# Kernel optimization log

Measured on AMD Instinct MI355X. Metric: run time of the kernel, lower is better.

## Reference

```python
import jax, jax.numpy as jnp
import numpy as np
from functools import partial

B, C, H, W = 256, 3, 128, 128

def _conv(x, w, b, pad):
    y = jax.lax.conv_general_dilated(x, w, (1, 1), [(pad, pad), (pad, pad)],
                                     dimension_numbers=('NCHW', 'OIHW', 'NCHW'))
    return y + b[None, :, None, None]

def _maxpool2(x):
    return jax.lax.reduce_window(x, -jnp.inf, jax.lax.max, (1, 1, 2, 2), (1, 1, 2, 2), 'VALID')

def _linear(x, w, b):
    return x @ w.T + b

def _handcrafted(images):
    # uint8 quantization: floor(x*255); inputs in [0,1) so no wraparound
    img8 = jnp.floor(images * 255.0)                      # [B,3,H,W]
    brightness = img8.mean(axis=(-2, -1))                 # [B,3]
    contrast = img8.std(axis=(-2, -1))                    # [B,3] (ddof=0, numpy default)
    # cv2.Sobel ksize=3, BORDER_REFLECT_101 == jnp.pad 'reflect'; cv2 does correlation
    kx = jnp.array([[-1., 0., 1.], [-2., 0., 2.], [-1., 0., 1.]], dtype=img8.dtype)
    ky = kx.T
    k = jnp.stack([kx, ky])[:, None]                      # [2,1,3,3]
    p = jnp.pad(img8, ((0, 0), (0, 0), (1, 1), (1, 1)), mode='reflect')
    s = jax.lax.conv_general_dilated(p.reshape(B * 3, 1, H + 2, W + 2), k, (1, 1),
                                     'VALID', dimension_numbers=('NCHW', 'OIHW', 'NCHW'))
    edge = jnp.sqrt(s[:, 0] ** 2 + s[:, 1] ** 2).mean(axis=(-2, -1)).reshape(B, 3)
    return jnp.concatenate([edge, brightness, contrast], axis=1)  # [B,9]

def setup_inputs() -> dict:
    key = jax.random.key(0)
    ks = jax.random.split(key, 20)
    g = lambda i, shape, fan: (jax.random.normal(ks[i], shape, jnp.float32) * (1.0 / np.sqrt(fan)))
    return {
        'images': jax.random.uniform(ks[0], (B, C, H, W), jnp.float32),
        'W1': g(1, (32, 3, 3, 3), 27), 'b1': jnp.zeros((32,), jnp.float32),
        'W2': g(2, (64, 32, 3, 3), 288), 'b2': jnp.zeros((64,), jnp.float32),
        'Wa': g(3, (1, 64, 7, 7), 64 * 49), 'ba': jnp.zeros((1,), jnp.float32),
        'Wfc': g(4, (50, 64 * 32 * 32), 64 * 32 * 32), 'bfc': jnp.zeros((50,), jnp.float32),
        'Wh1': g(5, (32, 9), 9), 'bh1': jnp.zeros((32,), jnp.float32),
        'Wh2': g(6, (64, 32), 32), 'bh2': jnp.zeros((64,), jnp.float32),
        'Wh3': g(7, (50, 64), 64), 'bh3': jnp.zeros((50,), jnp.float32),
        'Wf': g(8, (64, 100), 100), 'bf': jnp.zeros((64,), jnp.float32),
        'Wc': g(9, (1, 64), 64), 'bc': jnp.zeros((1,), jnp.float32),
    }

def reference(images, W1, b1, W2, b2, Wa, ba, Wfc, bfc,
              Wh1, bh1, Wh2, bh2, Wh3, bh3, Wf, bf, Wc, bc):
    # CNN branch
    x = jax.nn.relu(_conv(images, W1, b1, 1))
    x = _maxpool2(x)
    x = jax.nn.relu(_conv(x, W2, b2, 1))
    x = _maxpool2(x)                                      # [B,64,32,32]
    attn = jax.nn.sigmoid(_conv(x, Wa, ba, 3))            # spatial attention
    x = x * attn
    cnn_feat = jax.nn.relu(_linear(x.reshape(B, -1), Wfc, bfc))  # [B,50]
    # handcrafted branch
    f = _handcrafted(images)                              # [B,9]
    h = jax.nn.relu(_linear(f, Wh1, bh1))
    h = jax.nn.relu(_linear(h, Wh2, bh2))
    h = jax.nn.relu(_linear(h, Wh3, bh3))                 # [B,50]
    fused = jax.nn.relu(_linear(jnp.concatenate([cnn_feat, h], axis=1), Wf, bf))
    logits = _linear(fused, Wc, bc)
    return jax.nn.sigmoid(logits)
```

## Files before the change

kernel.cpp:

```cpp
#include <hip/hip_runtime.h>
#include <stdint.h>

typedef __bf16 bf16x8 __attribute__((ext_vector_type(8)));
typedef float f32x4 __attribute__((ext_vector_type(4)));

__device__ inline float bf2f(uint16_t u) {
    uint32_t x = ((uint32_t)u) << 16;
    float f;
    __builtin_memcpy(&f, &x, 4);
    return f;
}
__device__ inline uint16_t f2bf(float f) {
    uint32_t x;
    __builtin_memcpy(&x, &f, 4);
    uint32_t r = (x + 0x7FFFu + ((x >> 16) & 1u)) >> 16;
    return (uint16_t)r;
}

__global__ __launch_bounds__(256) void k_prep_w2(const float* __restrict__ W2,
                                                 uint16_t* __restrict__ wA) {
    int j = blockIdx.x * 256 + threadIdx.x;
    if (j >= 18432) return;
    int t = j >> 11, rem = j & 2047, oc = rem >> 5, ic = rem & 31;
    int dy = t / 3, dx = t - dy * 3;
    wA[j] = f2bf(W2[(oc * 32 + ic) * 9 + dy * 3 + dx]);
}

__global__ __launch_bounds__(256) void k_prep_w1(const float* __restrict__ W1,
                                                 uint16_t* __restrict__ wA1c) {
    int j = blockIdx.x * 256 + threadIdx.x;
    if (j >= 3072) return;
    int dy = j >> 10, rem = j & 1023, oc = rem >> 5, k = rem & 31;
    int dx = k >> 2, ic = k & 3;
    uint16_t v = 0;
    if (dx < 3 && ic < 3) v = f2bf(W1[((oc * 3 + ic) * 3 + dy) * 3 + dx]);
    wA1c[j] = v;
}

__global__ __launch_bounds__(256) void k_prep_wa(const float* __restrict__ Wa,
                                                 uint16_t* __restrict__ waP) {
    int j = blockIdx.x * 256 + threadIdx.x;
    if (j >= 4096) return;
    int chunk = j >> 10, ks = (j >> 9) & 1, tl = (j >> 5) & 15, ch = j & 31;
    int t = chunk * 16 + tl;
    int cg = ks * 32 + ch;
    waP[j] = (t < 49) ? f2bf(Wa[cg * 49 + t]) : (uint16_t)0;
}

__global__ __launch_bounds__(256) void k_prep_wfc(const float* __restrict__ Wfc,
                                                  uint16_t* __restrict__ wfcb) {
    int o = blockIdx.x;
    int pb = blockIdx.y;
    int ch = threadIdx.x & 63;
    int pr = threadIdx.x >> 6;
    const float* src = Wfc + (size_t)o * 65536 + ch * 1024;
    uint16_t* dst = wfcb + (size_t)o * 65536 + ch;
#pragma unroll 4
    for (int i = 0; i < 16; ++i) {
        int px = pb * 64 + i * 4 + pr;
        dst[(size_t)px * 64] = f2bf(src[px]);
    }
}

__global__ __launch_bounds__(256) void k_handcrafted(const float* __restrict__ img,
                                                     float* __restrict__ f) {
    __shared__ float p[128 * 128];
    int c = blockIdx.x, b = blockIdx.y;
    const float* src = img + (((size_t)(b * 3 + c)) << 14);
    int tid = threadIdx.x;
    float sum = 0.f, sumsq = 0.f;
    for (int it = 0; it < 64; ++it) {
        int idx = tid + (it << 8);
        float v = floorf(src[idx] * 255.0f);
        p[idx] = v;
        sum += v;
        sumsq += v * v;
    }
    __syncthreads();
    float esum = 0.f;
    for (int it = 0; it < 64; ++it) {
        int idx = tid + (it << 8);
        int r = idx >> 7, cc = idx & 127;
        int rm = (r == 0) ? 1 : (r - 1), rp = (r == 127) ? 126 : (r + 1);
        int cm = (cc == 0) ? 1 : (cc - 1), cp = (cc == 127) ? 126 : (cc + 1);
        float a0 = p[(rm << 7) + cm], a1 = p[(rm << 7) + cc], a2 = p[(rm << 7) + cp];
        float b0 = p[(r << 7) + cm], b2 = p[(r << 7) + cp];
        float c0 = p[(rp << 7) + cm], c1 = p[(rp << 7) + cc], c2 = p[(rp << 7) + cp];
        float gx = (a2 - a0) + 2.f * (b2 - b0) + (c2 - c0);
        float gy = (c0 + 2.f * c1 + c2) - (a0 + 2.f * a1 + a2);
        esum += sqrtf(gx * gx + gy * gy);
    }
    for (int off = 32; off; off >>= 1) {
        sum += __shfl_down(sum, off);
        sumsq += __shfl_down(sumsq, off);
        esum += __shfl_down(esum, off);
    }
    __syncthreads();
    int w = tid >> 6;
    if ((tid & 63) == 0) {
        p[w * 3 + 0] = sum;
        p[w * 3 + 1] = sumsq;
        p[w * 3 + 2] = esum;
    }
    __syncthreads();
    if (tid == 0) {
        float S = 0.f, Q = 0.f, E = 0.f;
        for (int i = 0; i < 4; ++i) {
            S += p[i * 3 + 0];
            Q += p[i * 3 + 1];
            E += p[i * 3 + 2];
        }
        const float inv = 1.0f / 16384.0f;
        float mean = S * inv;
        float var = Q * inv - mean * mean;
        f[b * 16 + c] = E * inv;
        f[b * 16 + 3 + c] = mean;
        f[b * 16 + 6 + c] = sqrtf(fmaxf(var, 0.f));
    }
}

__global__ __launch_bounds__(256) void k_conv1_mfma(const float* __restrict__ img,
                                                    const uint16_t* __restrict__ wA1c,
                                                    const float* __restrict__ b1,
                                                    uint16_t* __restrict__ pooled1) {
    __shared__ uint16_t s_nhwc[18 * 34 * 4 + 32];
    __shared__ uint16_t s_out[8 * 16 * 32];
    const int tile = blockIdx.x;
    const int b = blockIdx.y;
    const int ty = tile >> 2, tx = tile & 3;
    const int Y0 = ty * 16, X0 = tx * 32;
    const int tid = threadIdx.x;

    for (int j = tid; j < 612; j += 256) {
        int r = j / 34, sc = j - r * 34;
        int gy = Y0 - 1 + r, gx = X0 - 1 + sc;
        uint16_t d[4] = {0, 0, 0, 0};
        if ((unsigned)gy < 128u && (unsigned)gx < 128u) {
            size_t base = (((size_t)b * 3) << 14) + (gy << 7) + gx;
#pragma unroll
            for (int ic = 0; ic < 3; ++ic) d[ic] = f2bf(img[base + ((size_t)ic << 14)]);
        }
        *(uint2*)&s_nhwc[j * 4] = *(uint2*)d;
    }

    const int wv = tid >> 6, lane = tid & 63;
    const int rowl = lane & 15, kg = lane >> 4;

    bf16x8 afr[3][2];
#pragma unroll
    for (int dy = 0; dy < 3; ++dy)
#pragma unroll
        for (int g = 0; g < 2; ++g)
            afr[dy][g] = *(const bf16x8*)(wA1c + dy * 1024 + (g * 16 + rowl) * 32 + kg * 8);
    float bias[2][4];
#pragma unroll
    for (int g = 0; g < 2; ++g)
#pragma unroll
        for (int r = 0; r < 4; ++r)
            bias[g][r] = b1[g * 16 + kg * 4 + r];

    __syncthreads();

#pragma unroll
    for (int pr = 0; pr < 2; ++pr) {
#pragma unroll
        for (int seg = 0; seg < 2; ++seg) {
            const int y0 = wv * 4 + pr * 2;
            const int xl = seg * 16 + rowl;
            bf16x8 bw[4];
#pragma unroll
            for (int rr = 0; rr < 4; ++rr) {
                const uint16_t* rp = &s_nhwc[((y0 + rr) * 34 + xl + kg * 2) * 4];
                uint2 lo = *(const uint2*)rp;
                uint2 hi = *(const uint2*)(rp + 4);
                union { uint2 u[2]; bf16x8 v; } u;
                u.u[0] = lo;
                u.u[1] = hi;
                bw[rr] = u.v;
            }
            f32x4 acc0[2], acc1[2];
#pragma unroll
            for (int g = 0; g < 2; ++g)
#pragma unroll
                for (int r = 0; r < 4; ++r) {
                    acc0[g][r] = bias[g][r];
                    acc1[g][r] = bias[g][r];
                }
#pragma unroll
            for (int dy = 0; dy < 3; ++dy)
#pragma unroll
                for (int g = 0; g < 2; ++g) {
                    acc0[g] = __builtin_amdgcn_mfma_f32_16x16x32_bf16(afr[dy][g], bw[dy], acc0[g], 0, 0, 0);
                    acc1[g] = __builtin_amdgcn_mfma_f32_16x16x32_bf16(afr[dy][g], bw[dy + 1], acc1[g], 0, 0, 0);
                }
#pragma unroll
            for (int g = 0; g < 2; ++g)
#pragma unroll
                for (int r = 0; r < 4; ++r) {
                    float m = fmaxf(acc0[g][r], acc1[g][r]);
                    m = fmaxf(m, 0.f);
                    float o = fmaxf(m, __shfl_xor(m, 1));
                    if (!(lane & 1)) {
                        int prow = wv * 2 + pr;
                        int pcol = seg * 8 + (rowl >> 1);
                        int oc = g * 16 + kg * 4 + r;
                        s_out[(prow * 16 + pcol) * 32 + oc] = f2bf(o);
                    }
                }
        }
    }
    __syncthreads();
    for (int u = tid; u < 512; u += 256) {
        int px = u >> 2, c = u & 3;
        int prow = px >> 4, pcol = px & 15;
        uint4 v = *(const uint4*)&s_out[px * 32 + c * 8];
        ((uint4*)pooled1)[((((size_t)b << 12) + (ty * 8 + prow) * 64 + tx * 16 + pcol) << 2) + c] = v;
    }
}

__global__ __launch_bounds__(256) void k_conv2_mfma(const uint16_t* __restrict__ pooled1,
                                                    const uint16_t* __restrict__ wA,
                                                    const float* __restrict__ b2v,
                                                    uint16_t* __restrict__ pooled2n) {
    __shared__ uint16_t s_in[10 * 34 * 32];
    __shared__ uint16_t s_out[64 * 64];
    const int bx = blockIdx.x;
    const int b = blockIdx.y;
    const int tx = bx >> 3, ty = bx & 7;
    const int X0 = tx * 32, Y0 = ty * 8;
    const int tid = threadIdx.x;

    for (int j = tid; j < 1360; j += 256) {
        int r = j / 136;
        int rem = j - r * 136;
        int px = rem >> 2, c4 = rem & 3;
        int gy = Y0 - 1 + r, gx = X0 - 1 + px;
        uint4 v = make_uint4(0, 0, 0, 0);
        if ((unsigned)gy < 64u && (unsigned)gx < 64u)
            v = ((const uint4*)pooled1)[((((size_t)b << 12) + gy * 64 + gx) << 2) + c4];
        *(uint4*)&s_in[(r * 34 + px) * 32 + c4 * 8] = v;
    }

    const int wv = tid >> 6, lane = tid & 63;
    const int ocq = wv & 1, xth = wv >> 1;
    const int rowl = lane & 15, kg = lane >> 4;

    bf16x8 afr[9][2];
#pragma unroll
    for (int t = 0; t < 9; ++t)
#pragma unroll
        for (int g = 0; g < 2; ++g)
            afr[t][g] = *(const bf16x8*)(wA + t * 2048 + (ocq * 32 + g * 16 + rowl) * 32 + kg * 8);
    float bias[2][4];
#pragma unroll
    for (int g = 0; g < 2; ++g)
#pragma unroll
        for (int r = 0; r < 4; ++r)
            bias[g][r] = b2v[ocq * 32 + g * 16 + kg * 4 + r];

    __syncthreads();

    for (int yp = 0; yp < 4; ++yp) {
        f32x4 acc[2][2];
#pragma unroll
        for (int p = 0; p < 2; ++p)
#pragma unroll
            for (int g = 0; g < 2; ++g)
#pragma unroll
                for (int r = 0; r < 4; ++r) acc[p][g][r] = bias[g][r];

        bf16x8 bfr[4][3];
#pragma unroll
        for (int rr = 0; rr < 4; ++rr)
#pragma unroll
            for (int dx = 0; dx < 3; ++dx) {
                int pix = (2 * yp + rr) * 34 + xth * 16 + rowl + dx;
                bfr[rr][dx] = *(const bf16x8*)(s_in + pix * 32 + kg * 8);
            }
#pragma unroll
        for (int dy = 0; dy < 3; ++dy)
#pragma unroll
            for (int dx = 0; dx < 3; ++dx) {
                int t = dy * 3 + dx;
#pragma unroll
                for (int g = 0; g < 2; ++g) {
                    acc[0][g] = __builtin_amdgcn_mfma_f32_16x16x32_bf16(afr[t][g], bfr[dy][dx], acc[0][g], 0, 0, 0);
                    acc[1][g] = __builtin_amdgcn_mfma_f32_16x16x32_bf16(afr[t][g], bfr[dy + 1][dx], acc[1][g], 0, 0, 0);
                }
            }
#pragma unroll
        for (int g = 0; g < 2; ++g)
#pragma unroll
            for (int r = 0; r < 4; ++r) {
                float m = fmaxf(acc[0][g][r], acc[1][g][r]);
                m = fmaxf(m, 0.f);
                float o = fmaxf(m, __shfl_xor(m, 1));
                if (!(lane & 1)) {
                    int oc = ocq * 32 + g * 16 + kg * 4 + r;
                    int pxl = xth * 8 + (rowl >> 1);
                    int pl = yp * 16 + pxl;
                    s_out[pl * 64 + (oc ^ ((pxl & 7) << 3))] = f2bf(o);
                }
            }
    }
    __syncthreads();
    const int PY0 = ty * 4, PX0 = tx * 16;
    for (int u = tid; u < 512; u += 256) {
        int pl = u >> 3, c = u & 7;
        int py = pl >> 4, pxl = pl & 15;
        uint4 v = *(const uint4*)&s_out[pl * 64 + ((c ^ (pxl & 7)) << 3)];
        *(uint4*)&pooled2n[((((size_t)b << 10) + (PY0 + py) * 32 + PX0 + pxl) << 6) + c * 8] = v;
    }
}

__global__ __launch_bounds__(256) void k_attn_gemm(const uint16_t* __restrict__ pooled2n,
                                                   const uint16_t* __restrict__ waP,
                                                   const float* __restrict__ ba,
                                                   float* __restrict__ attn) {
    __shared__ uint16_t P[448 * 70];
    const int qt = blockIdx.x;
    const int b = blockIdx.y;
    const int tid = threadIdx.x;
    const int R0 = qt * 8;
    const int wv = tid >> 6, lane = tid & 63;
    const int rowl = lane & 15, kg = lane >> 4;

    bf16x8 afr[4][2];
#pragma unroll
    for (int c = 0; c < 4; ++c)
#pragma unroll
        for (int ks = 0; ks < 2; ++ks)
            afr[c][ks] = *(const bf16x8*)(waP + ((c * 2 + ks) * 16 + rowl) * 32 + kg * 8);

    for (int nt = wv; nt < 28; nt += 4) {
        int hpx = nt * 16 + rowl;
        int hrow = hpx >> 5, hcol = hpx & 31;
        int gy = R0 - 3 + hrow;
        bf16x8 bf0, bf1;
        if ((unsigned)gy < 32u) {
            const uint16_t* src = pooled2n + ((((size_t)b << 10) + (gy << 5) + hcol) << 6);
            bf0 = *(const bf16x8*)(src + kg * 8);
            bf1 = *(const bf16x8*)(src + 32 + kg * 8);
        } else {
            union { uint4 u; bf16x8 v; } z;
            z.u = make_uint4(0, 0, 0, 0);
            bf0 = z.v;
            bf1 = z.v;
        }
        f32x4 acc[4];
#pragma unroll
        for (int c = 0; c < 4; ++c)
#pragma unroll
            for (int r = 0; r < 4; ++r) acc[c][r] = 0.f;
#pragma unroll
        for (int c = 0; c < 4; ++c) {
            acc[c] = __builtin_amdgcn_mfma_f32_16x16x32_bf16(afr[c][0], bf0, acc[c], 0, 0, 0);
            acc[c] = __builtin_amdgcn_mfma_f32_16x16x32_bf16(afr[c][1], bf1, acc[c], 0, 0, 0);
        }
#pragma unroll
        for (int c = 0; c < 4; ++c) {
            uint32_t lo = (uint32_t)f2bf(acc[c][0]) | ((uint32_t)f2bf(acc[c][1]) << 16);
            uint32_t hi = (uint32_t)f2bf(acc[c][2]) | ((uint32_t)f2bf(acc[c][3]) << 16);
            uint16_t* dst = &P[hpx * 70 + c * 16 + kg * 4];
            *(uint32_t*)dst = lo;
            *(uint32_t*)(dst + 2) = hi;
        }
    }
    __syncthreads();

    const int pyl = tid >> 5, px = tid & 31;
    float v = ba[0];
#pragma unroll
    for (int dy = 0; dy < 7; ++dy) {
        int hl = pyl + dy;
#pragma unroll
        for (int dx = 0; dx < 7; ++dx) {
            int qx = px + dx - 3;
            if ((unsigned)qx < 32u) v += bf2f(P[(hl * 32 + qx) * 70 + dy * 7 + dx]);
        }
    }
    attn[((size_t)b << 10) + qt * 256 + tid] = 1.f / (1.f + __expf(-v));
}

__global__ __launch_bounds__(256) void k_fc_mfma(const uint16_t* __restrict__ pooled2n,
                                                 const float* __restrict__ attn,
                                                 const uint16_t* __restrict__ wfcb,
                                                 float* __restrict__ partial) {
    __shared__ uint16_t xh[128 * 128];
    const int it = blockIdx.x;
    const int kc = blockIdx.y;
    const int b0 = it * 16;
    const int K0 = kc * 1024;
    const int tid = threadIdx.x;

    for (int j = tid; j < 2048; j += 256) {
        int im = j >> 7, k8 = j & 127;
        int bimg = b0 + im;
        int gk = K0 + k8 * 8;
        int px = gk >> 6, ch0 = gk & 63;
        uint4 pv = *(const uint4*)&pooled2n[((((size_t)bimg << 10) + px) << 6) + ch0];
        float a = attn[((size_t)bimg << 10) + px];
        uint16_t s[8];
        *(uint4*)s = pv;
        uint16_t d[8];
#pragma unroll
        for (int i = 0; i < 8; ++i) d[i] = f2bf(bf2f(s[i]) * a);
        *(uint4*)&xh[k8 * 128 + im * 8] = *(uint4*)d;
    }

    const int wv = tid >> 6, lane = tid & 63;
    const int rowl = lane & 15, kg = lane >> 4;
    const uint16_t* wbase = wfcb + (size_t)(wv * 16 + rowl) * 65536 + K0 + kg * 8;

    __syncthreads();

    f32x4 acc = {0.f, 0.f, 0.f, 0.f};
#pragma unroll 4
    for (int kk = 0; kk < 32; ++kk) {
        bf16x8 af = *(const bf16x8*)(wbase + kk * 32);
        bf16x8 bf = *(const bf16x8*)&xh[(kk * 4 + kg) * 128 + rowl * 8];
        acc = __builtin_amdgcn_mfma_f32_16x16x32_bf16(af, bf, acc, 0, 0, 0);
    }
    float* pp = &partial[(((size_t)kc * 256 + (b0 + rowl)) << 6) + wv * 16 + kg * 4];
    *(f32x4*)pp = acc;
}

__global__ __launch_bounds__(64) void k_head(const float* __restrict__ fbuf,
                                             const float* __restrict__ partial,
                                             const float* __restrict__ Wh1, const float* __restrict__ bh1,
                                             const float* __restrict__ Wh2, const float* __restrict__ bh2,
                                             const float* __restrict__ Wh3, const float* __restrict__ bh3,
                                             const float* __restrict__ bfc,
                                             const float* __restrict__ Wf, const float* __restrict__ bf_,
                                             const float* __restrict__ Wc, const float* __restrict__ bc,
                                             float* __restrict__ out) {
    __shared__ float fl[9];
    __shared__ float h1[32];
    __shared__ float h2[64];
    __shared__ float cat[100];
    int b = blockIdx.x;
    int l = threadIdx.x;
    if (l < 9) fl[l] = fbuf[b * 16 + l];
    __syncthreads();
    if (l < 32) {
        float a = bh1[l];
        for (int i = 0; i < 9; ++i) a += fl[i] * Wh1[l * 9 + i];
        h1[l] = fmaxf(a, 0.f);
    }
    __syncthreads();
    {
        float a = bh2[l];
        for (int i = 0; i < 32; ++i) a += h1[i] * Wh2[l * 32 + i];
        h2[l] = fmaxf(a, 0.f);
    }
    __syncthreads();
    if (l < 50) {
        float a = bh3[l];
        for (int i = 0; i < 64; ++i) a += h2[i] * Wh3[l * 64 + i];
        cat[50 + l] = fmaxf(a, 0.f);
        float s = bfc[l];
        for (int kc2 = 0; kc2 < 64; ++kc2) s += partial[(((size_t)kc2 * 256 + b) << 6) + l];
        cat[l] = fmaxf(s, 0.f);
    }
    __syncthreads();
    float a = bf_[l];
    for (int i = 0; i < 100; ++i) a += cat[i] * Wf[l * 100 + i];
    a = fmaxf(a, 0.f);
    float v = a * Wc[l];
    for (int off = 32; off; off >>= 1) v += __shfl_down(v, off);
    if (l == 0) out[b] = 1.f / (1.f + __expf(-(v + bc[0])));
}

extern "C" void kernel_launch(void* const* d_in, const int* in_sizes, int n_in,
                              void* d_out, int out_size, void* d_ws, size_t ws_size,
                              hipStream_t stream) {
    const float* images = (const float*)d_in[0];
    const float* W1 = (const float*)d_in[1];
    const float* b1 = (const float*)d_in[2];
    const float* W2 = (const float*)d_in[3];
    const float* b2 = (const float*)d_in[4];
    const float* Wa = (const float*)d_in[5];
    const float* ba = (const float*)d_in[6];
    const float* Wfc = (const float*)d_in[7];
    const float* bfc = (const float*)d_in[8];
    const float* Wh1 = (const float*)d_in[9];
    const float* bh1 = (const float*)d_in[10];
    const float* Wh2 = (const float*)d_in[11];
    const float* bh2 = (const float*)d_in[12];
    const float* Wh3 = (const float*)d_in[13];
    const float* bh3 = (const float*)d_in[14];
    const float* Wf = (const float*)d_in[15];
    const float* bf_ = (const float*)d_in[16];
    const float* Wc = (const float*)d_in[17];
    const float* bc = (const float*)d_in[18];

    const size_t NEEDED = 102828032;
    if (ws_size < NEEDED) return;

    char* ws = (char*)d_ws;
    uint16_t* pooled1 = (uint16_t*)ws;
    uint16_t* pooled2n = (uint16_t*)(ws + 67108864);
    float* attn = (float*)(ws + 100663296);
    float* fbuf = (float*)(ws + 101711872);
    uint16_t* wA = (uint16_t*)(ws + 102776832);
    uint16_t* wA1c = (uint16_t*)(ws + 102813696);
    uint16_t* waP = (uint16_t*)(ws + 102819840);
    uint16_t* wfcb = (uint16_t*)ws;
    float* partial = (float*)(ws + 16777216);
    float* out = (float*)d_out;

    hipLaunchKernelGGL(k_prep_w2, dim3(72), dim3(256), 0, stream, W2, wA);
    hipLaunchKernelGGL(k_prep_w1, dim3(12), dim3(256), 0, stream, W1, wA1c);
    hipLaunchKernelGGL(k_prep_wa, dim3(16), dim3(256), 0, stream, Wa, waP);
    hipLaunchKernelGGL(k_handcrafted, dim3(3, 256), dim3(256), 0, stream, images, fbuf);
    hipLaunchKernelGGL(k_conv1_mfma, dim3(32, 256), dim3(256), 0, stream, images, wA1c, b1, pooled1);
    hipLaunchKernelGGL(k_conv2_mfma, dim3(16, 256), dim3(256), 0, stream, pooled1, wA, b2, pooled2n);
    hipLaunchKernelGGL(k_prep_wfc, dim3(50, 16), dim3(256), 0, stream, Wfc, wfcb);
    hipLaunchKernelGGL(k_attn_gemm, dim3(4, 256), dim3(256), 0, stream, pooled2n, waP, ba, attn);
    hipLaunchKernelGGL(k_fc_mfma, dim3(16, 64), dim3(256), 0, stream, pooled2n, attn, wfcb, partial);
    hipLaunchKernelGGL(k_head, dim3(256), dim3(64), 0, stream, fbuf, partial,
                       Wh1, bh1, Wh2, bh2, Wh3, bh3, bfc, Wf, bf_, Wc, bc, out);
}
```

Measured before the change: 182.1 us.

## Merge weight-prep kernels, slide Sobel window, restructure conv2 row reuse

Fuses three small weight-conversion kernels into one launch to cut launch overhead. The Sobel pass now has each thread sweep half a row with a sliding 3x3 register window over a padded shared array (stride 129), which reduces shared-memory loads and bank conflicts. conv2 loads each input row once and accumulates into all eight output-row accumulators, with launch_bounds min-blocks set to 2. In exchange conv2 holds more accumulator registers, and the Sobel loop has less thread parallelism and a serial dependency chain.

```diff
diff --git a/kernel.cpp b/kernel.cpp
--- a/kernel.cpp
+++ b/kernel.cpp
@@ -17,34 +17,36 @@
     return (uint16_t)r;
 }
 
-__global__ __launch_bounds__(256) void k_prep_w2(const float* __restrict__ W2,
-                                                 uint16_t* __restrict__ wA) {
-    int j = blockIdx.x * 256 + threadIdx.x;
-    if (j >= 18432) return;
-    int t = j >> 11, rem = j & 2047, oc = rem >> 5, ic = rem & 31;
-    int dy = t / 3, dx = t - dy * 3;
-    wA[j] = f2bf(W2[(oc * 32 + ic) * 9 + dy * 3 + dx]);
-}
-
-__global__ __launch_bounds__(256) void k_prep_w1(const float* __restrict__ W1,
-                                                 uint16_t* __restrict__ wA1c) {
-    int j = blockIdx.x * 256 + threadIdx.x;
-    if (j >= 3072) return;
-    int dy = j >> 10, rem = j & 1023, oc = rem >> 5, k = rem & 31;
-    int dx = k >> 2, ic = k & 3;
-    uint16_t v = 0;
-    if (dx < 3 && ic < 3) v = f2bf(W1[((oc * 3 + ic) * 3 + dy) * 3 + dx]);
-    wA1c[j] = v;
-}
-
-__global__ __launch_bounds__(256) void k_prep_wa(const float* __restrict__ Wa,
-                                                 uint16_t* __restrict__ waP) {
-    int j = blockIdx.x * 256 + threadIdx.x;
-    if (j >= 4096) return;
-    int chunk = j >> 10, ks = (j >> 9) & 1, tl = (j >> 5) & 15, ch = j & 31;
-    int t = chunk * 16 + tl;
-    int cg = ks * 32 + ch;
-    waP[j] = (t < 49) ? f2bf(Wa[cg * 49 + t]) : (uint16_t)0;
+__global__ __launch_bounds__(256) void k_prep_small(const float* __restrict__ W2,
+                                                    const float* __restrict__ W1,
+                                                    const float* __restrict__ Wa,
+                                                    uint16_t* __restrict__ wA,
+                                                    uint16_t* __restrict__ wA1c,
+                                                    uint16_t* __restrict__ waP) {
+    int bid = blockIdx.x;
+    int tid = threadIdx.x;
+    if (bid < 72) {
+        int j = bid * 256 + tid;
+        if (j >= 18432) return;
+        int t = j >> 11, rem = j & 2047, oc = rem >> 5, ic = rem & 31;
+        int dy = t / 3, dx = t - dy * 3;
+        wA[j] = f2bf(W2[(oc * 32 + ic) * 9 + dy * 3 + dx]);
+    } else if (bid < 84) {
+        int j = (bid - 72) * 256 + tid;
+        if (j >= 3072) return;
+        int dy = j >> 10, rem = j & 1023, oc = rem >> 5, k = rem & 31;
+        int dx = k >> 2, ic = k & 3;
+        uint16_t v = 0;
+        if (dx < 3 && ic < 3) v = f2bf(W1[((oc * 3 + ic) * 3 + dy) * 3 + dx]);
+        wA1c[j] = v;
+    } else {
+        int j = (bid - 84) * 256 + tid;
+        if (j >= 4096) return;
+        int chunk = j >> 10, ks = (j >> 9) & 1, tl = (j >> 5) & 15, ch = j & 31;
+        int t = chunk * 16 + tl;
+        int cg = ks * 32 + ch;
+        waP[j] = (t < 49) ? f2bf(Wa[cg * 49 + t]) : (uint16_t)0;
+    }
 }
 
 __global__ __launch_bounds__(256) void k_prep_wfc(const float* __restrict__ Wfc,
@@ -64,58 +66,85 @@
 
 __global__ __launch_bounds__(256) void k_handcrafted(const float* __restrict__ img,
                                                      float* __restrict__ f) {
-    __shared__ float p[128 * 128];
+    __shared__ float p[128 * 129];
     int c = blockIdx.x, b = blockIdx.y;
     const float* src = img + (((size_t)(b * 3 + c)) << 14);
     int tid = threadIdx.x;
     float sum = 0.f, sumsq = 0.f;
     for (int it = 0; it < 64; ++it) {
         int idx = tid + (it << 8);
+        int r = idx >> 7, cc = idx & 127;
         float v = floorf(src[idx] * 255.0f);
-        p[idx] = v;
+        p[r * 129 + cc] = v;
         sum += v;
         sumsq += v * v;
     }
     __syncthreads();
-    float esum = 0.f;
-    for (int it = 0; it < 64; ++it) {
-        int idx = tid + (it << 8);
-        int r = idx >> 7, cc = idx & 127;
+    {
+        int r = tid >> 1;
+        int c0 = (tid & 1) * 64;
         int rm = (r == 0) ? 1 : (r - 1), rp = (r == 127) ? 126 : (r + 1);
-        int cm = (cc == 0) ? 1 : (cc - 1), cp = (cc == 127) ? 126 : (cc + 1);
-        float a0 = p[(rm << 7) + cm], a1 = p[(rm << 7) + cc], a2 = p[(rm << 7) + cp];
-        float b0 = p[(r << 7) + cm], b2 = p[(r << 7) + cp];
-        float c0 = p[(rp << 7) + cm], c1 = p[(rp << 7) + cc], c2 = p[(rp << 7) + cp];
-        float gx = (a2 - a0) + 2.f * (b2 - b0) + (c2 - c0);
-        float gy = (c0 + 2.f * c1 + c2) - (a0 + 2.f * a1 + a2);
-        esum += sqrtf(gx * gx + gy * gy);
-    }
-    for (int off = 32; off; off >>= 1) {
-        sum += __shfl_down(sum, off);
-        sumsq += __shfl_down(sumsq, off);
-        esum += __shfl_down(esum, off);
-    }
-    __syncthreads();
-    int w = tid >> 6;
-    if ((tid & 63) == 0) {
-        p[w * 3 + 0] = sum;
-        p[w * 3 + 1] = sumsq;
-        p[w * 3 + 2] = esum;
-    }
-    __syncthreads();
-    if (tid == 0) {
-        float S = 0.f, Q = 0.f, E = 0.f;
-        for (int i = 0; i < 4; ++i) {
-            S += p[i * 3 + 0];
-            Q += p[i * 3 + 1];
-            E += p[i * 3 + 2];
-        }
-        const float inv = 1.0f / 16384.0f;
-        float mean = S * inv;
-        float var = Q * inv - mean * mean;
-        f[b * 16 + c] = E * inv;
-        f[b * 16 + 3 + c] = mean;
-        f[b * 16 + 6 + c] = sqrtf(fmaxf(var, 0.f));
+        const float* Pm = &p[rm * 129];
+        const float* P0 = &p[r * 129];
+        const float* Pp = &p[rp * 129];
+        float am, a0, ap, bm, b0, bp, cm, c0v, cp;
+        if (c0 == 0) {
+            a0 = Pm[0]; ap = Pm[1]; am = ap;
+            b0 = P0[0]; bp = P0[1]; bm = bp;
+            c0v = Pp[0]; cp = Pp[1]; cm = cp;
+        } else {
+            am = Pm[63]; a0 = Pm[64]; ap = Pm[65];
+            bm = P0[63]; b0 = P0[64]; bp = P0[65];
+            cm = Pp[63]; c0v = Pp[64]; cp = Pp[65];
+        }
+        float esum = 0.f;
+        for (int i = 0; i < 64; ++i) {
+            float gx = (ap - am) + 2.f * (bp - bm) + (cp - cm);
+            float gy = (cm + 2.f * c0v + cp) - (am + 2.f * a0 + ap);
+            esum += sqrtf(gx * gx + gy * gy);
+            if (i < 63) {
+                int nc = c0 + i + 2;
+                am = a0; a0 = ap;
+                bm = b0; b0 = bp;
+                cm = c0v; c0v = cp;
+                if (nc <= 127) {
+                    ap = Pm[nc];
+                    bp = P0[nc];
+                    cp = Pp[nc];
+                } else {
+                    ap = am;
+                    bp = bm;
+                    cp = cm;
+                }
+            }
+        }
+        for (int off = 32; off; off >>= 1) {
+            sum += __shfl_down(sum, off);
+            sumsq += __shfl_down(sumsq, off);
+            esum += __shfl_down(esum, off);
+        }
+        __syncthreads();
+        int w = tid >> 6;
+        if ((tid & 63) == 0) {
+            p[w * 3 + 0] = sum;
+            p[w * 3 + 1] = sumsq;
+            p[w * 3 + 2] = esum;
+        }
+        __syncthreads();
+        if (tid == 0) {
+            float S = 0.f, Q = 0.f, E = 0.f;
+            for (int i = 0; i < 4; ++i) {
+                S += p[i * 3 + 0];
+                Q += p[i * 3 + 1];
+                E += p[i * 3 + 2];
+            }
+            const float inv = 1.0f / 16384.0f;
+            float mean = S * inv;
+            float var = Q * inv - mean * mean;
+            f[b * 16 + c] = E * inv;
+            f[b * 16 + 3 + c] = mean;
+            f[b * 16 + 6 + c] = sqrtf(fmaxf(var, 0.f));
+        }
     }
 }
 
@@ -218,10 +247,10 @@
     }
 }
 
-__global__ __launch_bounds__(256) void k_conv2_mfma(const uint16_t* __restrict__ pooled1,
-                                                    const uint16_t* __restrict__ wA,
-                                                    const float* __restrict__ b2v,
-                                                    uint16_t* __restrict__ pooled2n) {
+__global__ __launch_bounds__(256, 2) void k_conv2_mfma(const uint16_t* __restrict__ pooled1,
+                                                       const uint16_t* __restrict__ wA,
+                                                       const float* __restrict__ b2v,
+                                                       uint16_t* __restrict__ pooled2n) {
     __shared__ uint16_t s_in[10 * 34 * 32];
     __shared__ uint16_t s_out[64 * 64];
     const int bx = blockIdx.x;
@@ -251,54 +280,61 @@
 #pragma unroll
         for (int g = 0; g < 2; ++g)
             afr[t][g] = *(const bf16x8*)(wA + t * 2048 + (ocq * 32 + g * 16 + rowl) * 32 + kg * 8);
-    float bias[2][4];
-#pragma unroll
-    for (int g = 0; g < 2; ++g)
-#pragma unroll
-        for (int r = 0; r < 4; ++r)
-            bias[g][r] = b2v[ocq * 32 + g * 16 + kg * 4 + r];
-
-    __syncthreads();
-
-    for (int yp = 0; yp < 4; ++yp) {
-        f32x4 acc[2][2];
-#pragma unroll
-        for (int p = 0; p < 2; ++p)
+
+    f32x4 acc[8][2];
+    {
+        float bias[2][4];
+#pragma unroll
+        for (int g = 0; g < 2; ++g)
+#pragma unroll
+            for (int r = 0; r < 4; ++r)
+                bias[g][r] = b2v[ocq * 32 + g * 16 + kg * 4 + r];
+#pragma unroll
+        for (int y = 0; y < 8; ++y)
 #pragma unroll
             for (int g = 0; g < 2; ++g)
 #pragma unroll
-                for (int r = 0; r < 4; ++r) acc[p][g][r] = bias[g][r];
-
-        bf16x8 bfr[4][3];
-#pragma unroll
-        for (int rr = 0; rr < 4; ++rr)
-#pragma unroll
-            for (int dx = 0; dx < 3; ++dx) {
-                int pix = (2 * yp + rr) * 34 + xth * 16 + rowl + dx;
-                bfr[rr][dx] = *(const bf16x8*)(s_in + pix * 32 + kg * 8);
-            }
-#pragma unroll
-        for (int dy = 0; dy < 3; ++dy)
-#pragma unroll
-            for (int dx = 0; dx < 3; ++dx) {
-                int t = dy * 3 + dx;
-#pragma unroll
-                for (int g = 0; g < 2; ++g) {
-                    acc[0][g] = __builtin_amdgcn_mfma_f32_16x16x32_bf16(afr[t][g], bfr[dy][dx], acc[0][g], 0, 0, 0);
-                    acc[1][g] = __builtin_amdgcn_mfma_f32_16x16x32_bf16(afr[t][g], bfr[dy + 1][dx], acc[1][g], 0, 0, 0);
+                for (int r = 0; r < 4; ++r) acc[y][g][r] = bias[g][r];
+    }
+
+    __syncthreads();
+
+#pragma unroll
+    for (int r = 0; r < 10; ++r) {
+        bf16x8 R[3];
+#pragma unroll
+        for (int dx = 0; dx < 3; ++dx) {
+            int pix = r * 34 + xth * 16 + rowl + dx;
+            R[dx] = *(const bf16x8*)(s_in + pix * 32 + kg * 8);
+        }
+#pragma unroll
+        for (int dyp = 0; dyp < 3; ++dyp) {
+            const int y = r - dyp;
+            if (y >= 0 && y < 8) {
+#pragma unroll
+                for (int dx = 0; dx < 3; ++dx) {
+                    const int t = dyp * 3 + dx;
+#pragma unroll
+                    for (int g = 0; g < 2; ++g)
+                        acc[y][g] = __builtin_amdgcn_mfma_f32_16x16x32_bf16(afr[t][g], R[dx], acc[y][g], 0, 0, 0);
                 }
             }
+        }
+    }
+
+#pragma unroll
+    for (int py = 0; py < 4; ++py) {
 #pragma unroll
         for (int g = 0; g < 2; ++g)
 #pragma unroll
-            for (int r = 0; r < 4; ++r) {
-                float m = fmaxf(acc[0][g][r], acc[1][g][r]);
+            for (int rr = 0; rr < 4; ++rr) {
+                float m = fmaxf(acc[2 * py][g][rr], acc[2 * py + 1][g][rr]);
                 m = fmaxf(m, 0.f);
                 float o = fmaxf(m, __shfl_xor(m, 1));
                 if (!(lane & 1)) {
-                    int oc = ocq * 32 + g * 16 + kg * 4 + r;
+                    int oc = ocq * 32 + g * 16 + kg * 4 + rr;
                     int pxl = xth * 8 + (rowl >> 1);
-                    int pl = yp * 16 + pxl;
+                    int pl = py * 16 + pxl;
                     s_out[pl * 64 + (oc ^ ((pxl & 7) << 3))] = f2bf(o);
                 }
             }
@@ -509,9 +545,7 @@
     float* partial = (float*)(ws + 16777216);
     float* out = (float*)d_out;
 
-    hipLaunchKernelGGL(k_prep_w2, dim3(72), dim3(256), 0, stream, W2, wA);
-    hipLaunchKernelGGL(k_prep_w1, dim3(12), dim3(256), 0, stream, W1, wA1c);
-    hipLaunchKernelGGL(k_prep_wa, dim3(16), dim3(256), 0, stream, Wa, waP);
+    hipLaunchKernelGGL(k_prep_small, dim3(100), dim3(256), 0, stream, W2, W1, Wa, wA, wA1c, waP);
     hipLaunchKernelGGL(k_handcrafted, dim3(3, 256), dim3(256), 0, stream, images, fbuf);
     hipLaunchKernelGGL(k_conv1_mfma, dim3(32, 256), dim3(256), 0, stream, images, wA1c, b1, pooled1);
     hipLaunchKernelGGL(k_conv2_mfma, dim3(16, 256), dim3(256), 0, stream, pooled1, wA, b2, pooled2n);
```

After: 179.5 us. No clear change (-1.5%).
